# Optimization experiments

Hardware: AMD Instinct MI355X
Metric: run time of the kernel (lower is better)

The kernel has to match this reference:

```python
import jax, jax.numpy as jnp
import numpy as np
from jax import lax

N = 256  # insize == outsize, must be even


def setup_inputs() -> dict:
    key = jax.random.key(0)
    k1, k2, k3 = jax.random.split(key, 3)
    x = jax.random.normal(k1, (65536, N), dtype=jnp.float32)
    # OrthogonalLinear: U = triu(randn(n, n))
    U = jnp.triu(jax.random.normal(k2, (N, N), dtype=jnp.float32))
    # theta init: 2*pi*rand; gamma init: ones
    theta = 2.0 * jnp.pi * jax.random.uniform(k3, (N // 2,), dtype=jnp.float32)
    gamma = jnp.ones((N // 2,), dtype=jnp.float32)
    return {"x": x, "U": U, "theta": theta, "gamma": gamma}


def _apply_P(M, U):
    """Householder product: for i in range(n): M = Hprod(M, U[i], n - i).
    Hprod only touches the last k = n - i entries, i.e. indices >= i; we
    express that by masking U[i] (exactly equivalent math since masked
    entries contribute 0 to the dot product and the update)."""
    n = U.shape[0]
    idx = jnp.arange(n)

    def step(xc, i):
        u = jnp.where(idx >= i, U[i], 0.0)            # [n]
        alpha = 2.0 * (xc @ u) / jnp.dot(u, u)        # [rows]
        xc = xc - alpha[:, None] * u[None, :]
        return xc, None

    out, _ = lax.scan(step, M, jnp.arange(n))
    return out


def _build_T(theta, gamma):
    """Block-diagonal T with 2x2 blocks gamma_k * R(theta_k)."""
    m = theta.shape[0]
    c = gamma * jnp.cos(theta)
    s = gamma * jnp.sin(theta)
    blocks = jnp.stack([jnp.stack([c, -s], -1), jnp.stack([s, c], -1)], -2)  # [m,2,2]
    T4 = jnp.zeros((m, 2, m, 2), dtype=theta.dtype)
    k = jnp.arange(m)
    T4 = T4.at[k, :, k, :].set(blocks)
    return T4.reshape(2 * m, 2 * m)


def reference(x, U, theta, gamma):
    n = U.shape[0]
    T = _build_T(theta, gamma)                 # [n, n]
    PT = _apply_P(T, U)                        # P(T)
    PW = _apply_P(jnp.eye(n, dtype=U.dtype), U)  # P.effective_W()
    W = PT @ PW.T                              # effective_W, [n, n]
    return x @ W                               # bias=False
```

## Files before the change

kernel.cpp:

```cpp
#include <hip/hip_runtime.h>
#include <math.h>


#define NCOLS 256
#define NPAIR (NCOLS / 2)
#define F4_PER_ROW (NCOLS / 4)

__global__ __launch_bounds__(256) void schur_rot_kernel(
    const float4* __restrict__ x4,
    const float* __restrict__ theta,
    const float* __restrict__ gamma,
    float4* __restrict__ out4,
    int total4)
{
    __shared__ float sc[NPAIR];
    __shared__ float ss[NPAIR];

    int t = threadIdx.x;
    if (t < NPAIR) {
        float th = theta[t];
        float g  = gamma[t];
        sc[t] = g * cosf(th);
        ss[t] = g * sinf(th);
    }
    __syncthreads();

    int idx = blockIdx.x * blockDim.x + t;
    if (idx >= total4) return;

    int col4 = idx & (F4_PER_ROW - 1);
    int k0 = 2 * col4;
    float c0 = sc[k0],     s0 = ss[k0];
    float c1 = sc[k0 + 1], s1 = ss[k0 + 1];

    float4 v = x4[idx];
    float4 o;
    o.x = c0 * v.x + s0 * v.y;
    o.y = c0 * v.y - s0 * v.x;
    o.z = c1 * v.z + s1 * v.w;
    o.w = c1 * v.w - s1 * v.z;
    out4[idx] = o;
}

extern "C" void kernel_launch(void* const* d_in, const int* in_sizes, int n_in,
                              void* d_out, int out_size, void* d_ws, size_t ws_size,
                              hipStream_t stream) {
    const float* x     = (const float*)d_in[0];
    const float* theta = (const float*)d_in[2];
    const float* gamma = (const float*)d_in[3];
    float* out = (float*)d_out;

    int total  = in_sizes[0];
    int total4 = total / 4;

    int block = 256;
    int grid  = (total4 + block - 1) / block;

    schur_rot_kernel<<<grid, block, 0, stream>>>(
        (const float4*)x, theta, gamma, (float4*)out, total4);
}
```

Measured before the change: 116.3 us.

## Use persistent grid-stride loop with per-thread rotation coefficients and 4x unroll

Replaces the one-float4-per-thread launch with a fixed grid of at most 2048 blocks running a grid-stride loop unrolled by four. Because the stride is a multiple of the row width in float4s, each thread's column stays fixed. Each thread therefore computes its own two cos/sin pairs once with sincosf, which drops the shared-memory table and the block barrier. The aim is to cut per-block setup and keep more loads in flight for this purely bandwidth-bound rotation. The cost is redundant trig work per thread and possibly less latency hiding if the fixed grid underfills the device.

```diff
diff --git a/kernel.cpp b/kernel.cpp
--- a/kernel.cpp
+++ b/kernel.cpp
@@ -3,7 +3,6 @@
 
 
 #define NCOLS 256
-#define NPAIR (NCOLS / 2)
 #define F4_PER_ROW (NCOLS / 4)
 
 __global__ __launch_bounds__(256) void schur_rot_kernel(
@@ -13,33 +12,58 @@
     float4* __restrict__ out4,
     int total4)
 {
-    __shared__ float sc[NPAIR];
-    __shared__ float ss[NPAIR];
+    int tid = blockIdx.x * blockDim.x + threadIdx.x;
+    int stride = gridDim.x * blockDim.x;
 
-    int t = threadIdx.x;
-    if (t < NPAIR) {
-        float th = theta[t];
-        float g  = gamma[t];
-        sc[t] = g * cosf(th);
-        ss[t] = g * sinf(th);
+    int col4 = tid & (F4_PER_ROW - 1);
+    int k0 = 2 * col4;
+
+    float s0, c0, s1, c1;
+    sincosf(theta[k0],     &s0, &c0);
+    sincosf(theta[k0 + 1], &s1, &c1);
+    float g0 = gamma[k0], g1 = gamma[k0 + 1];
+    c0 *= g0; s0 *= g0;
+    c1 *= g1; s1 *= g1;
+
+    int idx = tid;
+    for (; idx + 3 * stride < total4; idx += 4 * stride) {
+        float4 v0 = x4[idx];
+        float4 v1 = x4[idx + stride];
+        float4 v2 = x4[idx + 2 * stride];
+        float4 v3 = x4[idx + 3 * stride];
+
+        float4 o0, o1, o2, o3;
+        o0.x = fmaf(c0, v0.x,  s0 * v0.y);
+        o0.y = fmaf(c0, v0.y, -s0 * v0.x);
+        o0.z = fmaf(c1, v0.z,  s1 * v0.w);
+        o0.w = fmaf(c1, v0.w, -s1 * v0.z);
+        o1.x = fmaf(c0, v1.x,  s0 * v1.y);
+        o1.y = fmaf(c0, v1.y, -s0 * v1.x);
+        o1.z = fmaf(c1, v1.z,  s1 * v1.w);
+        o1.w = fmaf(c1, v1.w, -s1 * v1.z);
+        o2.x = fmaf(c0, v2.x,  s0 * v2.y);
+        o2.y = fmaf(c0, v2.y, -s0 * v2.x);
+        o2.z = fmaf(c1, v2.z,  s1 * v2.w);
+        o2.w = fmaf(c1, v2.w, -s1 * v2.z);
+        o3.x = fmaf(c0, v3.x,  s0 * v3.y);
+        o3.y = fmaf(c0, v3.y, -s0 * v3.x);
+        o3.z = fmaf(c1, v3.z,  s1 * v3.w);
+        o3.w = fmaf(c1, v3.w, -s1 * v3.z);
+
+        out4[idx]              = o0;
+        out4[idx + stride]     = o1;
+        out4[idx + 2 * stride] = o2;
+        out4[idx + 3 * stride] = o3;
     }
-    __syncthreads();
-
-    int idx = blockIdx.x * blockDim.x + t;
-    if (idx >= total4) return;
-
-    int col4 = idx & (F4_PER_ROW - 1);
-    int k0 = 2 * col4;
-    float c0 = sc[k0],     s0 = ss[k0];
-    float c1 = sc[k0 + 1], s1 = ss[k0 + 1];
-
-    float4 v = x4[idx];
-    float4 o;
-    o.x = c0 * v.x + s0 * v.y;
-    o.y = c0 * v.y - s0 * v.x;
-    o.z = c1 * v.z + s1 * v.w;
-    o.w = c1 * v.w - s1 * v.z;
-    out4[idx] = o;
+    for (; idx < total4; idx += stride) {
+        float4 v = x4[idx];
+        float4 o;
+        o.x = fmaf(c0, v.x,  s0 * v.y);
+        o.y = fmaf(c0, v.y, -s0 * v.x);
+        o.z = fmaf(c1, v.z,  s1 * v.w);
+        o.w = fmaf(c1, v.w, -s1 * v.z);
+        out4[idx] = o;
+    }
 }
 
 extern "C" void kernel_launch(void* const* d_in, const int* in_sizes, int n_in,
@@ -54,7 +78,9 @@
     int total4 = total / 4;
 
     int block = 256;
-    int grid  = (total4 + block - 1) / block;
+    int grid  = 2048;
+    int maxgrid = (total4 + block - 1) / block;
+    if (grid > maxgrid) grid = maxgrid;
 
     schur_rot_kernel<<<grid, block, 0, stream>>>(
         (const float4*)x, theta, gamma, (float4*)out, total4);
```

Result: no change. 117.5 us (+1.1%).
